# Performance work log

Hardware: AMD Instinct MI355X
Metric: run time of the kernel (lower is better)

## Reference

```python
import jax, jax.numpy as jnp
import numpy as np

EPS = 1e-5

def conv1d(x, w, b, pad):
    # x: [N, Cin, T], w: [Cout, Cin, K]
    y = jax.lax.conv_general_dilated(x, w, (1,), [(pad, pad)],
                                     dimension_numbers=("NCH", "OIH", "NCH"))
    return y + b[None, :, None]

def bn_eval(x, gamma, beta, mean, var):
    # BatchNorm1d in inference mode over channel dim of [N, C, T]
    inv = gamma / jnp.sqrt(var + EPS)
    return x * inv[None, :, None] + (beta - mean * inv)[None, :, None]

def setup_inputs() -> dict:
    key = jax.random.key(0)
    ks = jax.random.split(key, 16)
    B, E, N, T = 8, 16, 64, 128
    D, OUT = 32, 64  # timeseries_dim, output_dim
    inp = {
        "node_features": jax.random.normal(ks[0], (B, E, N, T, 1), dtype=jnp.float32),
        "edge_features": jax.random.normal(ks[1], (B, E, T), dtype=jnp.float32),
        "conv1_w": jax.random.normal(ks[2], (D, 1, 3), dtype=jnp.float32) * 0.3,
        "conv1_b": jax.random.normal(ks[3], (D,), dtype=jnp.float32) * 0.1,
        "conv2_w": jax.random.normal(ks[4], (1, D, 3), dtype=jnp.float32) * 0.1,
        "conv2_b": jax.random.normal(ks[5], (1,), dtype=jnp.float32) * 0.1,
        "conv3_w": jax.random.normal(ks[6], (OUT, 1, 1), dtype=jnp.float32) * 0.3,
        "conv3_b": jax.random.normal(ks[7], (OUT,), dtype=jnp.float32) * 0.1,
        "bn1_gamma": jax.random.uniform(ks[8], (D,), dtype=jnp.float32) + 0.5,
        "bn1_beta": jax.random.normal(ks[9], (D,), dtype=jnp.float32) * 0.1,
        "bn1_mean": jax.random.normal(ks[10], (D,), dtype=jnp.float32) * 0.1,
        "bn1_var": jax.random.uniform(ks[11], (D,), dtype=jnp.float32) + 0.5,
        "bn2_gamma": jax.random.uniform(ks[12], (1,), dtype=jnp.float32) + 0.5,
        "bn2_beta": jax.random.normal(ks[13], (1,), dtype=jnp.float32) * 0.1,
        "bn2_mean": jax.random.normal(ks[14], (1,), dtype=jnp.float32) * 0.1,
        "bn2_var": jax.random.uniform(ks[15], (1,), dtype=jnp.float32) + 0.5,
    }
    return inp

def reference(node_features, edge_features, conv1_w, conv1_b, conv2_w, conv2_b,
              conv3_w, conv3_b, bn1_gamma, bn1_beta, bn1_mean, bn1_var,
              bn2_gamma, bn2_beta, bn2_mean, bn2_var):
    B, E, N, T, _ = node_features.shape
    OUT = conv3_w.shape[0]
    # Self-connectivity: each (b,e,n) node processes its own [1,1,T] series and
    # the sum over its (single) connected edge is the identity. Fuse the triple
    # python loop into one batched conv pipeline over B*E*N series.
    x = node_features.reshape(B * E * N, 1, T)          # [BEN, 1, T]
    x = jax.nn.relu(bn_eval(conv1d(x, conv1_w, conv1_b, 1),
                            bn1_gamma, bn1_beta, bn1_mean, bn1_var))  # [BEN, D, T]
    x = jax.nn.relu(bn_eval(conv1d(x, conv2_w, conv2_b, 1),
                            bn2_gamma, bn2_beta, bn2_mean, bn2_var))  # [BEN, 1, T]
    x = conv1d(x, conv3_w, conv3_b, 0)                  # [BEN, OUT, T]
    return x.reshape(B, E, N, OUT, T)
```

## Files before the change

### kernel.cpp

```cpp
#include <hip/hip_runtime.h>

#define EPSF 1e-5f
#define SER 4

typedef float f32x4 __attribute__((ext_vector_type(4)));


__global__ __launch_bounds__(128) void hnc_kernel(
    const float* __restrict__ x_in,
    const float* __restrict__ w1,
    const float* __restrict__ b1,
    const float* __restrict__ w2,
    const float* __restrict__ b2,
    const float* __restrict__ w3,
    const float* __restrict__ b3,
    const float* __restrict__ g1, const float* __restrict__ be1,
    const float* __restrict__ m1, const float* __restrict__ v1,
    const float* __restrict__ g2, const float* __restrict__ be2,
    const float* __restrict__ m2, const float* __restrict__ v2,
    float* __restrict__ out)
{
    __shared__ float x_s[2][132];
    __shared__ float y2_s[2][128];
    __shared__ f32x4 pkA_s[32];
    __shared__ f32x4 pkB_s[32];
    __shared__ float w3_s[64];
    __shared__ float b3_s[64];
    __shared__ float c2_s;

    const int tid = threadIdx.x;
    const size_t s0 = (size_t)blockIdx.x * SER;

    x_s[0][2 + tid] = x_in[s0 * 128 + tid];
    if (tid < 2)      { x_s[0][tid] = 0.f;       x_s[1][tid] = 0.f; }
    else if (tid < 4) { x_s[0][128 + tid] = 0.f; x_s[1][128 + tid] = 0.f; }

    if (tid < 32) {
        const int d = tid;
        float inv = g1[d] * rsqrtf(v1[d] + EPSF);
        f32x4 A;
        A.x = inv * w1[d * 3 + 0];
        A.y = inv * w1[d * 3 + 1];
        A.z = inv * w1[d * 3 + 2];
        A.w = b1[d] * inv + be1[d] - m1[d] * inv;
        pkA_s[d] = A;
    } else if (tid < 64) {
        const int d = tid - 32;
        float s2 = g2[0] * rsqrtf(v2[0] + EPSF);
        f32x4 W;
        W.x = s2 * w2[d * 3 + 0];
        W.y = s2 * w2[d * 3 + 1];
        W.z = s2 * w2[d * 3 + 2];
        W.w = 0.f;
        pkB_s[d] = W;
        if (d == 0) c2_s = b2[0] * s2 + be2[0] - m2[0] * s2;
    } else {
        const int o = tid - 64;
        w3_s[o] = w3[o];
        b3_s[o] = b3[o];
    }
    __syncthreads();

    const float mm = (tid == 0)   ? 0.f : 1.f;
    const float mp = (tid == 127) ? 0.f : 1.f;
    const int   og = tid >> 5;
    const int   ty = (tid << 2) & 127;

    for (int s = 0; s < SER; ++s) {
        const int cur = s & 1, nxt = cur ^ 1;

        float xpre = 0.f;
        if (s + 1 < SER) xpre = x_in[(s0 + s + 1) * 128 + tid];

        const float xm2 = x_s[cur][tid];
        const float xm1 = x_s[cur][tid + 1];
        const float x0  = x_s[cur][tid + 2];
        const float xp1 = x_s[cur][tid + 3];
        const float xp2 = x_s[cur][tid + 4];

        float accm = 0.f, acc0 = 0.f, accp = 0.f;
        #pragma unroll 4
        for (int d = 0; d < 32; ++d) {
            const f32x4 A = pkA_s[d];
            const f32x4 W = pkB_s[d];
            float ym = fmaxf(fmaf(A.x, xm2, fmaf(A.y, xm1, fmaf(A.z, x0,  A.w))), 0.f);
            float y0 = fmaxf(fmaf(A.x, xm1, fmaf(A.y, x0,  fmaf(A.z, xp1, A.w))), 0.f);
            float yp = fmaxf(fmaf(A.x, x0,  fmaf(A.y, xp1, fmaf(A.z, xp2, A.w))), 0.f);
            accm = fmaf(W.x, ym, accm);
            acc0 = fmaf(W.y, y0, acc0);
            accp = fmaf(W.z, yp, accp);
        }
        y2_s[cur][tid] = fmaxf(fmaf(mm, accm, fmaf(mp, accp, acc0 + c2_s)), 0.f);
        __syncthreads();

        const f32x4 y = *(const f32x4*)&y2_s[cur][ty];
        f32x4* out4 = (f32x4*)(out + (s0 + s) * 64 * 128);
        #pragma unroll
        for (int i = 0; i < 16; ++i) {
            const int o = 4 * i + og;
            const float w = w3_s[o], b = b3_s[o];
            f32x4 r;
            r.x = fmaf(w, y.x, b);
            r.y = fmaf(w, y.y, b);
            r.z = fmaf(w, y.z, b);
            r.w = fmaf(w, y.w, b);
            out4[i * 128 + tid] = r;
        }

        if (s + 1 < SER) {
            x_s[nxt][2 + tid] = xpre;
            __syncthreads();
        }
    }
}

extern "C" void kernel_launch(void* const* d_in, const int* in_sizes, int n_in,
                              void* d_out, int out_size, void* d_ws, size_t ws_size,
                              hipStream_t stream) {
    const float* x   = (const float*)d_in[0];
    const float* w1  = (const float*)d_in[2];
    const float* b1  = (const float*)d_in[3];
    const float* w2  = (const float*)d_in[4];
    const float* b2  = (const float*)d_in[5];
    const float* w3  = (const float*)d_in[6];
    const float* b3  = (const float*)d_in[7];
    const float* g1  = (const float*)d_in[8];
    const float* be1 = (const float*)d_in[9];
    const float* m1  = (const float*)d_in[10];
    const float* v1  = (const float*)d_in[11];
    const float* g2  = (const float*)d_in[12];
    const float* be2 = (const float*)d_in[13];
    const float* m2  = (const float*)d_in[14];
    const float* v2  = (const float*)d_in[15];

    const int T = 128;
    const int n_series = in_sizes[0] / T;
    const int n_blocks = n_series / SER;

    hnc_kernel<<<n_blocks, 128, 0, stream>>>(x, w1, b1, w2, b2, w3, b3,
                                             g1, be1, m1, v1, g2, be2, m2, v2,
                                             (float*)d_out);
}
```

Baseline: 50.83 us.

## Process all series per block together: batch input loads, share weight reads, single-phase store

Loads all four input series into shared memory up front. The conv1/conv2 inner loop now runs over all series at once, so each packed weight read from shared memory is reused four times. All outputs are then written in one store phase after a single barrier. This drops the per-series barriers and the serial compute-then-store alternation, which should let the stores of different series overlap and give more independent FMA chains. The cost is higher register pressure and a longer compute phase before any output store starts.

```diff
diff --git a/kernel.cpp b/kernel.cpp
--- a/kernel.cpp
+++ b/kernel.cpp
@@ -20,8 +20,8 @@
     const float* __restrict__ m2, const float* __restrict__ v2,
     float* __restrict__ out)
 {
-    __shared__ float x_s[2][132];
-    __shared__ float y2_s[2][128];
+    __shared__ float x_s[SER][132];
+    __shared__ float y2_s[SER][128];
     __shared__ f32x4 pkA_s[32];
     __shared__ f32x4 pkB_s[32];
     __shared__ float w3_s[64];
@@ -31,12 +31,16 @@
     const int tid = threadIdx.x;
     const size_t s0 = (size_t)blockIdx.x * SER;
 
-    x_s[0][2 + tid] = x_in[s0 * 128 + tid];
-    if (tid < 2)      { x_s[0][tid] = 0.f;       x_s[1][tid] = 0.f; }
-    else if (tid < 4) { x_s[0][128 + tid] = 0.f; x_s[1][128 + tid] = 0.f; }
+    #pragma unroll
+    for (int s = 0; s < SER; ++s)
+        x_s[s][2 + tid] = x_in[(s0 + s) * 128 + tid];
+    if (tid < SER) {
+        x_s[tid][0] = 0.f; x_s[tid][1] = 0.f;
+        x_s[tid][130] = 0.f; x_s[tid][131] = 0.f;
+    }
 
-    if (tid < 32) {
-        const int d = tid;
+    if (tid >= 32 && tid < 64) {
+        const int d = tid - 32;
         float inv = g1[d] * rsqrtf(v1[d] + EPSF);
         f32x4 A;
         A.x = inv * w1[d * 3 + 0];
@@ -44,8 +48,8 @@
         A.z = inv * w1[d * 3 + 2];
         A.w = b1[d] * inv + be1[d] - m1[d] * inv;
         pkA_s[d] = A;
-    } else if (tid < 64) {
-        const int d = tid - 32;
+    } else if (tid >= 64 && tid < 96) {
+        const int d = tid - 64;
         float s2 = g2[0] * rsqrtf(v2[0] + EPSF);
         f32x4 W;
         W.x = s2 * w2[d * 3 + 0];
@@ -54,46 +58,52 @@
         W.w = 0.f;
         pkB_s[d] = W;
         if (d == 0) c2_s = b2[0] * s2 + be2[0] - m2[0] * s2;
-    } else {
-        const int o = tid - 64;
-        w3_s[o] = w3[o];
-        b3_s[o] = b3[o];
+    } else if (tid >= 96) {
+        const int o = (tid - 96) * 2;
+        w3_s[o] = w3[o];     w3_s[o + 1] = w3[o + 1];
+        b3_s[o] = b3[o];     b3_s[o + 1] = b3[o + 1];
     }
     __syncthreads();
 
+    float xm2[SER], xm1[SER], x0[SER], xp1[SER], xp2[SER];
+    float accm[SER], acc0[SER], accp[SER];
+    #pragma unroll
+    for (int s = 0; s < SER; ++s) {
+        xm2[s] = x_s[s][tid];
+        xm1[s] = x_s[s][tid + 1];
+        x0[s]  = x_s[s][tid + 2];
+        xp1[s] = x_s[s][tid + 3];
+        xp2[s] = x_s[s][tid + 4];
+        accm[s] = 0.f; acc0[s] = 0.f; accp[s] = 0.f;
+    }
+
+    #pragma unroll 4
+    for (int d = 0; d < 32; ++d) {
+        const f32x4 A = pkA_s[d];
+        const f32x4 W = pkB_s[d];
+        #pragma unroll
+        for (int s = 0; s < SER; ++s) {
+            float ym = fmaxf(fmaf(A.x, xm2[s], fmaf(A.y, xm1[s], fmaf(A.z, x0[s],  A.w))), 0.f);
+            float y0 = fmaxf(fmaf(A.x, xm1[s], fmaf(A.y, x0[s],  fmaf(A.z, xp1[s], A.w))), 0.f);
+            float yp = fmaxf(fmaf(A.x, x0[s],  fmaf(A.y, xp1[s], fmaf(A.z, xp2[s], A.w))), 0.f);
+            accm[s] = fmaf(W.x, ym, accm[s]);
+            acc0[s] = fmaf(W.y, y0, acc0[s]);
+            accp[s] = fmaf(W.z, yp, accp[s]);
+        }
+    }
+
     const float mm = (tid == 0)   ? 0.f : 1.f;
     const float mp = (tid == 127) ? 0.f : 1.f;
-    const int   og = tid >> 5;
-    const int   ty = (tid << 2) & 127;
+    #pragma unroll
+    for (int s = 0; s < SER; ++s)
+        y2_s[s][tid] = fmaxf(fmaf(mm, accm[s], fmaf(mp, accp[s], acc0[s] + c2_s)), 0.f);
+    __syncthreads();
 
+    const int og = tid >> 5;
+    const int ty = (tid << 2) & 127;
+    #pragma unroll
     for (int s = 0; s < SER; ++s) {
-        const int cur = s & 1, nxt = cur ^ 1;
-
-        float xpre = 0.f;
-        if (s + 1 < SER) xpre = x_in[(s0 + s + 1) * 128 + tid];
-
-        const float xm2 = x_s[cur][tid];
-        const float xm1 = x_s[cur][tid + 1];
-        const float x0  = x_s[cur][tid + 2];
-        const float xp1 = x_s[cur][tid + 3];
-        const float xp2 = x_s[cur][tid + 4];
-
-        float accm = 0.f, acc0 = 0.f, accp = 0.f;
-        #pragma unroll 4
-        for (int d = 0; d < 32; ++d) {
-            const f32x4 A = pkA_s[d];
-            const f32x4 W = pkB_s[d];
-            float ym = fmaxf(fmaf(A.x, xm2, fmaf(A.y, xm1, fmaf(A.z, x0,  A.w))), 0.f);
-            float y0 = fmaxf(fmaf(A.x, xm1, fmaf(A.y, x0,  fmaf(A.z, xp1, A.w))), 0.f);
-            float yp = fmaxf(fmaf(A.x, x0,  fmaf(A.y, xp1, fmaf(A.z, xp2, A.w))), 0.f);
-            accm = fmaf(W.x, ym, accm);
-            acc0 = fmaf(W.y, y0, acc0);
-            accp = fmaf(W.z, yp, accp);
-        }
-        y2_s[cur][tid] = fmaxf(fmaf(mm, accm, fmaf(mp, accp, acc0 + c2_s)), 0.f);
-        __syncthreads();
-
-        const f32x4 y = *(const f32x4*)&y2_s[cur][ty];
+        const f32x4 y = *(const f32x4*)&y2_s[s][ty];
         f32x4* out4 = (f32x4*)(out + (s0 + s) * 64 * 128);
         #pragma unroll
         for (int i = 0; i < 16; ++i) {
@@ -105,11 +115,6 @@
             r.z = fmaf(w, y.z, b);
             r.w = fmaf(w, y.w, b);
             out4[i * 128 + tid] = r;
-        }
-
-        if (s + 1 < SER) {
-            x_s[nxt][2 + tid] = xpre;
-            __syncthreads();
         }
     }
 }
```

Result: no change. 50.49 us (-0.7%).

## Replace LDS exchange and barriers with wave shuffles, preload all series

Applied to the files above, without the earlier changes.

Loads all four input series into shared memory up front and removes the per-series double buffering and its barriers. The conv2 output is redistributed within each 64-lane wavefront with shuffles rather than through shared memory plus a block barrier. Each wave therefore writes only its own half of the time axis, which changes the mapping of threads to output channels and positions. The conv3 weights and biases are held in registers. This takes block-wide synchronisation out of the loop in exchange for more registers and more shuffle instructions.

```diff
diff --git a/kernel.cpp b/kernel.cpp
--- a/kernel.cpp
+++ b/kernel.cpp
@@ -20,21 +20,24 @@
     const float* __restrict__ m2, const float* __restrict__ v2,
     float* __restrict__ out)
 {
-    __shared__ float x_s[2][132];
-    __shared__ float y2_s[2][128];
+    __shared__ float x_s[SER][132];
     __shared__ f32x4 pkA_s[32];
     __shared__ f32x4 pkB_s[32];
     __shared__ float w3_s[64];
     __shared__ float b3_s[64];
     __shared__ float c2_s;
 
-    const int tid = threadIdx.x;
+    const int tid  = threadIdx.x;
+    const int lane = tid & 63;
     const size_t s0 = (size_t)blockIdx.x * SER;
 
-    x_s[0][2 + tid] = x_in[s0 * 128 + tid];
-    if (tid < 2)      { x_s[0][tid] = 0.f;       x_s[1][tid] = 0.f; }
-    else if (tid < 4) { x_s[0][128 + tid] = 0.f; x_s[1][128 + tid] = 0.f; }
-
+    #pragma unroll
+    for (int s = 0; s < SER; ++s)
+        x_s[s][2 + tid] = x_in[(s0 + s) * 128 + tid];
+    if (tid < SER) {
+        x_s[tid][0] = 0.f; x_s[tid][1] = 0.f;
+        x_s[tid][130] = 0.f; x_s[tid][131] = 0.f;
+    }
     if (tid < 32) {
         const int d = tid;
         float inv = g1[d] * rsqrtf(v1[d] + EPSF);
@@ -61,22 +64,25 @@
     }
     __syncthreads();
 
+    const int g  = lane >> 4;
+    const int qq = (tid >> 6) * 16 + (lane & 15);
+    const int srcl = 4 * (lane & 15);
+    float w3r[16], b3r[16];
+    #pragma unroll
+    for (int i = 0; i < 16; ++i) {
+        w3r[i] = w3_s[4 * i + g];
+        b3r[i] = b3_s[4 * i + g];
+    }
     const float mm = (tid == 0)   ? 0.f : 1.f;
     const float mp = (tid == 127) ? 0.f : 1.f;
-    const int   og = tid >> 5;
-    const int   ty = (tid << 2) & 127;
+    const float c2 = c2_s;
 
     for (int s = 0; s < SER; ++s) {
-        const int cur = s & 1, nxt = cur ^ 1;
-
-        float xpre = 0.f;
-        if (s + 1 < SER) xpre = x_in[(s0 + s + 1) * 128 + tid];
-
-        const float xm2 = x_s[cur][tid];
-        const float xm1 = x_s[cur][tid + 1];
-        const float x0  = x_s[cur][tid + 2];
-        const float xp1 = x_s[cur][tid + 3];
-        const float xp2 = x_s[cur][tid + 4];
+        const float xm2 = x_s[s][tid];
+        const float xm1 = x_s[s][tid + 1];
+        const float x0  = x_s[s][tid + 2];
+        const float xp1 = x_s[s][tid + 3];
+        const float xp2 = x_s[s][tid + 4];
 
         float accm = 0.f, acc0 = 0.f, accp = 0.f;
         #pragma unroll 4
@@ -90,26 +96,23 @@
             acc0 = fmaf(W.y, y0, acc0);
             accp = fmaf(W.z, yp, accp);
         }
-        y2_s[cur][tid] = fmaxf(fmaf(mm, accm, fmaf(mp, accp, acc0 + c2_s)), 0.f);
-        __syncthreads();
+        const float y2v = fmaxf(fmaf(mm, accm, fmaf(mp, accp, acc0 + c2)), 0.f);
 
-        const f32x4 y = *(const f32x4*)&y2_s[cur][ty];
+        f32x4 y;
+        y.x = __shfl(y2v, srcl + 0, 64);
+        y.y = __shfl(y2v, srcl + 1, 64);
+        y.z = __shfl(y2v, srcl + 2, 64);
+        y.w = __shfl(y2v, srcl + 3, 64);
+
         f32x4* out4 = (f32x4*)(out + (s0 + s) * 64 * 128);
         #pragma unroll
         for (int i = 0; i < 16; ++i) {
-            const int o = 4 * i + og;
-            const float w = w3_s[o], b = b3_s[o];
             f32x4 r;
-            r.x = fmaf(w, y.x, b);
-            r.y = fmaf(w, y.y, b);
-            r.z = fmaf(w, y.z, b);
-            r.w = fmaf(w, y.w, b);
-            out4[i * 128 + tid] = r;
-        }
-
-        if (s + 1 < SER) {
-            x_s[nxt][2 + tid] = xpre;
-            __syncthreads();
+            r.x = fmaf(w3r[i], y.x, b3r[i]);
+            r.y = fmaf(w3r[i], y.y, b3r[i]);
+            r.z = fmaf(w3r[i], y.z, b3r[i]);
+            r.w = fmaf(w3r[i], y.w, b3r[i]);
+            out4[(4 * i + g) * 32 + qq] = r;
         }
     }
 }
```

Measured after the change: 49.55 us. -2.5%, faster.
